# Kernel optimization log

Measured on AMD Instinct MI355X. Metric: run time of the kernel, lower is better.

The kernel has to match this reference:

```python
import jax, jax.numpy as jnp
import numpy as np

B, S, D_MODEL, N_HEAD = 8, 512, 1024, 16
HEAD_DIM = D_MODEL // N_HEAD


def _pos_embed(seq_len, dim):
    # RelativeSinusoidalPositionalEmbedding(dim, padding_idx=0, init_size=1200)
    num = 1201  # init_size + 1
    half = dim // 2
    freq = np.exp(np.arange(half, dtype=np.float32) * (-np.log(10000.0) / (half - 1)))
    pos = np.arange(-((num + 1) // 2), num // 2, dtype=np.float32)  # tf.range(-num//2, num//2), python floor div
    emb = pos[:, None] * freq[None, :]
    table = np.concatenate([np.sin(emb), np.cos(emb)], axis=1).astype(np.float32)  # [num, dim]
    table[0] = 0.0  # padding_idx = 0
    origin_shift = num // 2 + 1  # 601
    idx = np.arange(-seq_len, seq_len) + origin_shift
    return jnp.asarray(table[idx])  # [2*seq_len, dim]


def setup_inputs() -> dict:
    key = jax.random.key(0)
    k1, k2, k3, k4 = jax.random.split(key, 4)
    return {
        "x": jax.random.normal(k1, (B, S, D_MODEL), dtype=jnp.float32),
        "mask": jnp.ones((B, S), dtype=jnp.int32),
        "Wqv": jax.random.normal(k2, (D_MODEL, 2 * D_MODEL), dtype=jnp.float32) * 0.02,
        "r_r_bias": jax.random.normal(k3, (N_HEAD, HEAD_DIM), dtype=jnp.float32) * 0.02,
        "r_w_bias": jax.random.normal(k4, (N_HEAD, HEAD_DIM), dtype=jnp.float32) * 0.02,
    }


def _shift(BD):
    # [b, h, s, 2s] -> [b, h, s, s] via pad-reshape trick
    b, h, s, _ = BD.shape
    zp = jnp.zeros((b, h, s, 1), BD.dtype)
    BD = jnp.concatenate([BD, zp], axis=-1).reshape(b, h, 2 * s + 1, s)
    BD = BD[:, :, :-1].reshape(b, h, s, 2 * s)
    return BD[:, :, :, s:]


def reference(x, mask, Wqv, r_r_bias, r_w_bias):
    pos = _pos_embed(S, HEAD_DIM)  # [2S, head_dim], stop-gradient constant
    qv = x @ Wqv  # [B, S, 2*D]
    q, v = jnp.split(qv, 2, axis=-1)

    def heads(t):
        return t.reshape(B, S, N_HEAD, HEAD_DIM).transpose(0, 2, 1, 3)  # bhsd

    q, k, v = heads(q), heads(x), heads(v)
    rw_q = q + r_r_bias[None, :, None, :]
    AC = jnp.einsum('bhqd,bhkd->bhqk', rw_q, k)
    D_ = jnp.einsum('hd,ld->hl', r_w_bias, pos)[None, :, None, :]  # [1, h, 1, 2S]
    B_ = jnp.einsum('bhqd,ld->bhql', q, pos)  # [b, h, S, 2S]
    BD = _shift(B_ + D_)
    attn = AC + BD  # scale=False -> divide by 1
    m = mask.astype(jnp.float32)[:, None, None, :]
    attn = attn * m - (1.0 - m) * 1e8
    attn = jax.nn.softmax(attn, axis=-1)  # dropout is identity at inference
    out = jnp.einsum('bhqk,bhkd->bhqd', attn, v)
    return out.transpose(0, 2, 1, 3).reshape(B, S, D_MODEL)
```

## Files before the change

kernel.cpp:

```cpp
#include <hip/hip_runtime.h>


using h4 = __attribute__((ext_vector_type(4))) _Float16;
using h8 = __attribute__((ext_vector_type(8))) _Float16;
using f32x4 = __attribute__((ext_vector_type(4))) float;

#define MFMA16(a, b, c) __builtin_amdgcn_mfma_f32_16x16x32_f16((a), (b), (c), 0, 0, 0)

#define GLOAD_LDS16(gp, lp)                                                        \
  __builtin_amdgcn_global_load_lds(                                                \
      (const __attribute__((address_space(1))) unsigned int*)(gp),                 \
      (__attribute__((address_space(3))) unsigned int*)(lp), 16, 0, 0)

#define L2E 1.4426950408889634f

__global__ __launch_bounds__(256) void k_prep(const float* __restrict__ x,
                                              const float* __restrict__ Wqv,
                                              _Float16* __restrict__ xh,
                                              _Float16* __restrict__ wT,
                                              _Float16* __restrict__ posP) {
  __shared__ _Float16 t[64][72];
  int bid = blockIdx.x;
  int tid = threadIdx.x;
  if (bid < 2048) {
    size_t idx = (size_t)bid * 256 + tid;
    const float* src = x + idx * 8;
    _Float16 tmp[8];
#pragma unroll
    for (int j = 0; j < 8; ++j) tmp[j] = (_Float16)src[j];
    *(h8*)(xh + idx * 8) = *(const h8*)tmp;
  } else if (bid < 2176) {
    int idx = (bid - 2048) * 256 + tid;
    int tt = idx >> 6, j = idx & 63;
    int jj = j & 31;
    float f = expf((float)jj * (-9.210340371976184f / 31.0f));
    float ang = (float)tt * f;
    posP[idx] = (_Float16)((j < 32) ? sinf(ang) : cosf(ang));
  } else {
    int b2 = bid - 2176;
    int bk = b2 & 15, bn = b2 >> 4;
    int k0 = bk * 64, n0 = bn * 64;
    int r = tid >> 2, c = (tid & 3) * 16;
    const float* src = Wqv + (size_t)(k0 + r) * 2048 + n0 + c;
#pragma unroll
    for (int j = 0; j < 16; ++j) t[r][c + j] = (_Float16)src[j];
    __syncthreads();
    _Float16 tmp[16];
#pragma unroll
    for (int j = 0; j < 16; ++j) tmp[j] = t[c + j][r];
    _Float16* dst = wT + (size_t)(n0 + r) * 1024 + k0 + c;
    *(h8*)dst = *(const h8*)tmp;
    *(h8*)(dst + 8) = *(const h8*)(tmp + 8);
  }
}

__global__ __launch_bounds__(256) void k_gemm(const _Float16* __restrict__ xh,
                                              const _Float16* __restrict__ wT,
                                              const float* __restrict__ rr,
                                              const float* __restrict__ rw,
                                              _Float16* __restrict__ qrr,
                                              _Float16* __restrict__ qrwp,
                                              _Float16* __restrict__ vT) {
  __shared__ _Float16 At[2][128 * 64];
  __shared__ _Float16 Bt[2][128 * 64];

  int bid = blockIdx.x;
  int bm = bid & 31, bn = bid >> 5;
  int tid = threadIdx.x;
  int w = tid >> 6, lane = tid & 63;
  int lr = lane & 15, lg = lane >> 4;

  auto stage = [&](int bufi, int k0) {
#pragma unroll
    for (int it = 0; it < 4; ++it) {
      int a = w * 256 + it * 64 + lane;
      int trow = a >> 3, c8s = (a & 7) ^ (trow & 7);
      GLOAD_LDS16(xh + (size_t)(bm * 128 + trow) * 1024 + k0 + c8s * 8,
                  &At[bufi][a * 8]);
    }
#pragma unroll
    for (int it = 0; it < 4; ++it) {
      int a = w * 256 + it * 64 + lane;
      int trow = a >> 3, c8s = (a & 7) ^ (trow & 7);
      GLOAD_LDS16(wT + (size_t)(bn * 128 + trow) * 1024 + k0 + c8s * 8,
                  &Bt[bufi][a * 8]);
    }
  };

  int wm = w >> 1, wn = w & 1;
  f32x4 acc[4][4] = {};

  stage(0, 0);
  __syncthreads();
  int buf = 0;
  for (int i = 0; i < 16; ++i) {
    if (i < 15) stage(buf ^ 1, (i + 1) * 64);
#pragma unroll
    for (int kk = 0; kk < 2; ++kk) {
      h8 af[4], bf[4];
#pragma unroll
      for (int mi = 0; mi < 4; ++mi) {
        int row = wm * 64 + mi * 16 + lr;
        af[mi] = *(const h8*)(&At[buf][row * 64 + (((kk * 4 + lg) ^ (lr & 7)) * 8)]);
      }
#pragma unroll
      for (int ni = 0; ni < 4; ++ni) {
        int row = wn * 64 + ni * 16 + lr;
        bf[ni] = *(const h8*)(&Bt[buf][row * 64 + (((kk * 4 + lg) ^ (lr & 7)) * 8)]);
      }
#pragma unroll
      for (int mi = 0; mi < 4; ++mi)
#pragma unroll
        for (int ni = 0; ni < 4; ++ni)
          acc[mi][ni] = MFMA16(af[mi], bf[ni], acc[mi][ni]);
    }
    __syncthreads();
    buf ^= 1;
  }

  int hg = bn * 2 + wn;
  int mb = bm * 128 + wm * 64;
  if (hg < 16) {
    int h = hg;
    float rrv[4], rwv[4];
#pragma unroll
    for (int ni = 0; ni < 4; ++ni) {
      rrv[ni] = rr[h * 64 + ni * 16 + lr];
      rwv[ni] = rw[h * 64 + ni * 16 + lr];
    }
    float f0 = expf((float)lr * (-9.210340371976184f / 31.0f));
    float f1 = expf((float)(16 + lr) * (-9.210340371976184f / 31.0f));
#pragma unroll
    for (int mi = 0; mi < 4; ++mi)
#pragma unroll
      for (int r = 0; r < 4; ++r) {
        int m = mb + mi * 16 + lg * 4 + r;
        int b = m >> 9, s = m & 511;
        size_t base = ((size_t)(b * 16 + h) * 512 + s) * 64;
#pragma unroll
        for (int ni = 0; ni < 4; ++ni)
          qrr[base + ni * 16 + lr] = (_Float16)((acc[mi][ni][r] + rrv[ni]) * L2E);
        {
          float qs = acc[mi][0][r] + rwv[0], qc = acc[mi][2][r] + rwv[2];
          float sn, cs;
          __sincosf((float)s * f0, &sn, &cs);
          qrwp[base + lr] = (_Float16)((qs * cs + qc * sn) * L2E);
          qrwp[base + lr + 32] = (_Float16)((qc * cs - qs * sn) * L2E);
        }
        {
          float qs = acc[mi][1][r] + rwv[1], qc = acc[mi][3][r] + rwv[3];
          float sn, cs;
          __sincosf((float)s * f1, &sn, &cs);
          qrwp[base + 16 + lr] = (_Float16)((qs * cs + qc * sn) * L2E);
          qrwp[base + 16 + lr + 32] = (_Float16)((qc * cs - qs * sn) * L2E);
        }
      }
  } else {
    int h = hg - 16;
#pragma unroll
    for (int mi = 0; mi < 4; ++mi) {
      int m = mb + mi * 16 + lg * 4;
      int b = m >> 9, s0 = m & 511;
      size_t vtbase = (size_t)(b * 16 + h) * 64 * 512;
#pragma unroll
      for (int ni = 0; ni < 4; ++ni) {
        int d = ni * 16 + lr;
        _Float16 t4[4];
#pragma unroll
        for (int r = 0; r < 4; ++r) t4[r] = (_Float16)acc[mi][ni][r];
        *(h4*)(vT + vtbase + (size_t)d * 512 + s0) = *(const h4*)t4;
      }
    }
  }
}

__global__ __launch_bounds__(256, 2) void k_attn(const _Float16* __restrict__ xh,
                                                 const _Float16* __restrict__ qrr,
                                                 const _Float16* __restrict__ qrwp,
                                                 const _Float16* __restrict__ vT,
                                                 const _Float16* __restrict__ posPg,
                                                 const int* __restrict__ mask,
                                                 float* __restrict__ out) {
  __shared__ _Float16 Kp[128 * 128];
  __shared__ _Float16 Vt[64 * 128];
  __shared__ _Float16 Pl[4][16 * 136];
  __shared__ float Ma[512];

  int bid = blockIdx.x;
  int qb = bid >> 7, h = bid & 15, b = (bid >> 4) & 7;
  int q0 = qb * 128;
  int tid = threadIdx.x;
  int w = tid >> 6, lane = tid & 63;
  int lr = lane & 15, lg = lane >> 4;

  const size_t bh = (size_t)(b * 16 + h);
  const _Float16* kb = xh + (size_t)b * 512 * 1024 + h * 64;
  const _Float16* vTp = vT + bh * 64 * 512;
  const int* mrow = mask + b * 512;

  auto stage = [&](int t0s) {
#pragma unroll
    for (int it = 0; it < 8; ++it) {
      int a = w * 512 + it * 64 + lane;
      int trow = a >> 4, c16 = a & 15;
      int c16s = c16 ^ (trow & 15);
      const _Float16* g = (c16s < 8)
          ? kb + (size_t)(t0s + trow) * 1024 + c16s * 8
          : posPg + (size_t)(t0s + trow) * 64 + (c16s - 8) * 8;
      GLOAD_LDS16(g, &Kp[(size_t)(w * 512 + it * 64) * 8]);
    }
#pragma unroll
    for (int it = 0; it < 4; ++it) {
      int a = w * 256 + it * 64 + lane;
      int drow = a >> 4, c16 = a & 15;
      int c16s = c16 ^ (drow & 15);
      const _Float16* g = vTp + (size_t)drow * 512 + t0s + c16s * 8;
      GLOAD_LDS16(g, &Vt[(size_t)(w * 256 + it * 64) * 8]);
    }
  };

  Ma[tid] = (1.f - (float)mrow[tid]) * -1.4426950e8f;
  Ma[tid + 256] = (1.f - (float)mrow[tid + 256]) * -1.4426950e8f;

  h8 ar0[2], ar1[2], aw0[2], aw1[2];
#pragma unroll
  for (int rg = 0; rg < 2; ++rg) {
    const _Float16* qrr_p = qrr + (bh * 512 + q0 + 32 * w + 16 * rg + lr) * 64 + lg * 8;
    const _Float16* qrw_p = qrwp + (bh * 512 + q0 + 32 * w + 16 * rg + lr) * 64 + lg * 8;
    ar0[rg] = *(const h8*)(qrr_p);
    ar1[rg] = *(const h8*)(qrr_p + 32);
    aw0[rg] = *(const h8*)(qrw_p);
    aw1[rg] = *(const h8*)(qrw_p + 32);
  }

  float m_run[2] = {-1e30f, -1e30f}, l_run[2] = {0.f, 0.f};
  f32x4 O[2][4];
#pragma unroll
  for (int rg = 0; rg < 2; ++rg)
#pragma unroll
    for (int df = 0; df < 4; ++df) O[rg][df] = (f32x4){0.f, 0.f, 0.f, 0.f};

  _Float16* pw = &Pl[w][0];

  for (int t0 = 0; t0 < 512; t0 += 128) {
    stage(t0);
    __syncthreads();

#pragma unroll
    for (int rg = 0; rg < 2; ++rg) {
      float s[8][4];
      __builtin_amdgcn_s_setprio(1);
#pragma unroll
      for (int tf = 0; tf < 8; ++tf) {
        int row = tf * 16 + lr;
        const _Float16* bp = &Kp[row * 128];
        h8 b0 = *(const h8*)(bp + ((0 + lg) ^ lr) * 8);
        h8 b1 = *(const h8*)(bp + ((4 + lg) ^ lr) * 8);
        h8 b2 = *(const h8*)(bp + ((8 + lg) ^ lr) * 8);
        h8 b3 = *(const h8*)(bp + ((12 + lg) ^ lr) * 8);
        f32x4 c = {0.f, 0.f, 0.f, 0.f};
        c = MFMA16(b0, ar0[rg], c);
        c = MFMA16(b1, ar1[rg], c);
        c = MFMA16(b2, aw0[rg], c);
        c = MFMA16(b3, aw1[rg], c);
        f32x4 mav = *(const f32x4*)&Ma[t0 + tf * 16 + lg * 4];
#pragma unroll
        for (int r = 0; r < 4; ++r) s[tf][r] = c[r] + mav[r];
      }
      __builtin_amdgcn_s_setprio(0);

      float rm = s[0][0];
#pragma unroll
      for (int tf = 0; tf < 8; ++tf)
#pragma unroll
        for (int r = 0; r < 4; ++r) rm = fmaxf(rm, s[tf][r]);
      rm = fmaxf(rm, __shfl_xor(rm, 16));
      rm = fmaxf(rm, __shfl_xor(rm, 32));

      if (!__all(rm - m_run[rg] <= 8.f)) {
        float mn = fmaxf(m_run[rg], rm);
        float sc = exp2f(m_run[rg] - mn);
        m_run[rg] = mn;
        l_run[rg] *= sc;
        float scq[4];
#pragma unroll
        for (int r = 0; r < 4; ++r) scq[r] = __shfl(sc, lg * 4 + r);
#pragma unroll
        for (int df = 0; df < 4; ++df)
#pragma unroll
          for (int r = 0; r < 4; ++r) O[rg][df][r] *= scq[r];
      }

      float rs = 0.f;
#pragma unroll
      for (int tf = 0; tf < 8; ++tf) {
        _Float16 p4[4];
#pragma unroll
        for (int r = 0; r < 4; ++r) {
          float p = exp2f(s[tf][r] - m_run[rg]);
          p4[r] = (_Float16)p;
          rs += (float)p4[r];
        }
        *(h4*)(pw + lr * 136 + tf * 16 + lg * 4) = *(const h4*)p4;
      }
      rs += __shfl_xor(rs, 16);
      rs += __shfl_xor(rs, 32);
      l_run[rg] += rs;

      h8 pa[4];
#pragma unroll
      for (int ks = 0; ks < 4; ++ks)
        pa[ks] = *(const h8*)(pw + lr * 136 + ks * 32 + lg * 8);
      __builtin_amdgcn_s_setprio(1);
#pragma unroll
      for (int df = 0; df < 4; ++df) {
        int row = df * 16 + lr;
        const _Float16* vbp = &Vt[row * 128];
#pragma unroll
        for (int ks = 0; ks < 4; ++ks) {
          h8 vb = *(const h8*)(vbp + ((ks * 4 + lg) ^ lr) * 8);
          O[rg][df] = MFMA16(pa[ks], vb, O[rg][df]);
        }
      }
      __builtin_amdgcn_s_setprio(0);
    }
    __syncthreads();
  }

#pragma unroll
  for (int rg = 0; rg < 2; ++rg) {
    float lq[4];
#pragma unroll
    for (int r = 0; r < 4; ++r) lq[r] = __shfl(l_run[rg], lg * 4 + r);
#pragma unroll
    for (int df = 0; df < 4; ++df)
#pragma unroll
      for (int r = 0; r < 4; ++r) {
        int ii = 32 * w + 16 * rg + lg * 4 + r;
        out[((size_t)b * 512 + q0 + ii) * 1024 + h * 64 + df * 16 + lr] =
            O[rg][df][r] / lq[r];
      }
  }
}

extern "C" void kernel_launch(void* const* d_in, const int* in_sizes, int n_in,
                              void* d_out, int out_size, void* d_ws, size_t ws_size,
                              hipStream_t stream) {
  const float* x = (const float*)d_in[0];
  const int* mask = (const int*)d_in[1];
  const float* Wqv = (const float*)d_in[2];
  const float* rr = (const float*)d_in[3];
  const float* rw = (const float*)d_in[4];
  float* out = (float*)d_out;
  char* ws = (char*)d_ws;
  const size_t MB = 1024 * 1024;
  _Float16* xh = (_Float16*)(ws);
  _Float16* wT = (_Float16*)(ws + 8 * MB);
  _Float16* posP = (_Float16*)(ws + 12 * MB);
  _Float16* qrr = (_Float16*)(ws + 13 * MB);
  _Float16* qrwp = (_Float16*)(ws + 21 * MB);
  _Float16* vT = (_Float16*)(ws + 29 * MB);

  k_prep<<<2688, 256, 0, stream>>>(x, Wqv, xh, wT, posP);
  k_gemm<<<512, 256, 0, stream>>>(xh, wT, rr, rw, qrr, qrwp, vT);
  k_attn<<<512, 256, 0, stream>>>(xh, qrr, qrwp, vT, posP, mask, out);
}
```

Measured before the change: 67.74 us.

## Halve attention query tile, read V straight from global, raise occupancy

The attention kernel now gives each block 64 query rows instead of 128, so each wave handles one 16-row group. The grid doubles to 1024 blocks and launch bounds ask for 3 blocks per CU. The V tile is no longer staged in LDS; each wave loads its V fragments from global memory into registers, which frees LDS so more blocks can be resident. In exchange, every K/pos tile is staged into LDS for half as many queries, and each wave reads the full V tile on its own, which adds redundant global and cache traffic.

Result: slower. 111.9 us (+65.3%).

```diff
diff --git a/kernel.cpp b/kernel.cpp
--- a/kernel.cpp
+++ b/kernel.cpp
@@ -174,7 +174,7 @@
   }
 }
 
-__global__ __launch_bounds__(256, 2) void k_attn(const _Float16* __restrict__ xh,
+__global__ __launch_bounds__(256, 3) void k_attn(const _Float16* __restrict__ xh,
                                                  const _Float16* __restrict__ qrr,
                                                  const _Float16* __restrict__ qrwp,
                                                  const _Float16* __restrict__ vT,
@@ -182,13 +182,12 @@
                                                  const int* __restrict__ mask,
                                                  float* __restrict__ out) {
   __shared__ _Float16 Kp[128 * 128];
-  __shared__ _Float16 Vt[64 * 128];
   __shared__ _Float16 Pl[4][16 * 136];
   __shared__ float Ma[512];
 
   int bid = blockIdx.x;
   int qb = bid >> 7, h = bid & 15, b = (bid >> 4) & 7;
-  int q0 = qb * 128;
+  int q0 = qb * 64;
   int tid = threadIdx.x;
   int w = tid >> 6, lane = tid & 63;
   int lr = lane & 15, lg = lane >> 4;
@@ -209,36 +208,22 @@
           : posPg + (size_t)(t0s + trow) * 64 + (c16s - 8) * 8;
       GLOAD_LDS16(g, &Kp[(size_t)(w * 512 + it * 64) * 8]);
     }
-#pragma unroll
-    for (int it = 0; it < 4; ++it) {
-      int a = w * 256 + it * 64 + lane;
-      int drow = a >> 4, c16 = a & 15;
-      int c16s = c16 ^ (drow & 15);
-      const _Float16* g = vTp + (size_t)drow * 512 + t0s + c16s * 8;
-      GLOAD_LDS16(g, &Vt[(size_t)(w * 256 + it * 64) * 8]);
-    }
   };
 
   Ma[tid] = (1.f - (float)mrow[tid]) * -1.4426950e8f;
   Ma[tid + 256] = (1.f - (float)mrow[tid + 256]) * -1.4426950e8f;
 
-  h8 ar0[2], ar1[2], aw0[2], aw1[2];
-#pragma unroll
-  for (int rg = 0; rg < 2; ++rg) {
-    const _Float16* qrr_p = qrr + (bh * 512 + q0 + 32 * w + 16 * rg + lr) * 64 + lg * 8;
-    const _Float16* qrw_p = qrwp + (bh * 512 + q0 + 32 * w + 16 * rg + lr) * 64 + lg * 8;
-    ar0[rg] = *(const h8*)(qrr_p);
-    ar1[rg] = *(const h8*)(qrr_p + 32);
-    aw0[rg] = *(const h8*)(qrw_p);
-    aw1[rg] = *(const h8*)(qrw_p + 32);
-  }
-
-  float m_run[2] = {-1e30f, -1e30f}, l_run[2] = {0.f, 0.f};
-  f32x4 O[2][4];
-#pragma unroll
-  for (int rg = 0; rg < 2; ++rg)
-#pragma unroll
-    for (int df = 0; df < 4; ++df) O[rg][df] = (f32x4){0.f, 0.f, 0.f, 0.f};
+  const _Float16* qrr_p = qrr + (bh * 512 + q0 + 16 * w + lr) * 64 + lg * 8;
+  const _Float16* qrw_p = qrwp + (bh * 512 + q0 + 16 * w + lr) * 64 + lg * 8;
+  h8 ar0 = *(const h8*)(qrr_p);
+  h8 ar1 = *(const h8*)(qrr_p + 32);
+  h8 aw0 = *(const h8*)(qrw_p);
+  h8 aw1 = *(const h8*)(qrw_p + 32);
+
+  float m_run = -1e30f, l_run = 0.f;
+  f32x4 O[4];
+#pragma unroll
+  for (int df = 0; df < 4; ++df) O[df] = (f32x4){0.f, 0.f, 0.f, 0.f};
 
   _Float16* pw = &Pl[w][0];
 
@@ -246,101 +231,99 @@
     stage(t0);
     __syncthreads();
 
-#pragma unroll
-    for (int rg = 0; rg < 2; ++rg) {
-      float s[8][4];
-      __builtin_amdgcn_s_setprio(1);
-#pragma unroll
-      for (int tf = 0; tf < 8; ++tf) {
-        int row = tf * 16 + lr;
-        const _Float16* bp = &Kp[row * 128];
-        h8 b0 = *(const h8*)(bp + ((0 + lg) ^ lr) * 8);
-        h8 b1 = *(const h8*)(bp + ((4 + lg) ^ lr) * 8);
-        h8 b2 = *(const h8*)(bp + ((8 + lg) ^ lr) * 8);
-        h8 b3 = *(const h8*)(bp + ((12 + lg) ^ lr) * 8);
-        f32x4 c = {0.f, 0.f, 0.f, 0.f};
-        c = MFMA16(b0, ar0[rg], c);
-        c = MFMA16(b1, ar1[rg], c);
-        c = MFMA16(b2, aw0[rg], c);
-        c = MFMA16(b3, aw1[rg], c);
-        f32x4 mav = *(const f32x4*)&Ma[t0 + tf * 16 + lg * 4];
-#pragma unroll
-        for (int r = 0; r < 4; ++r) s[tf][r] = c[r] + mav[r];
-      }
-      __builtin_amdgcn_s_setprio(0);
-
-      float rm = s[0][0];
-#pragma unroll
-      for (int tf = 0; tf < 8; ++tf)
-#pragma unroll
-        for (int r = 0; r < 4; ++r) rm = fmaxf(rm, s[tf][r]);
-      rm = fmaxf(rm, __shfl_xor(rm, 16));
-      rm = fmaxf(rm, __shfl_xor(rm, 32));
-
-      if (!__all(rm - m_run[rg] <= 8.f)) {
-        float mn = fmaxf(m_run[rg], rm);
-        float sc = exp2f(m_run[rg] - mn);
-        m_run[rg] = mn;
-        l_run[rg] *= sc;
-        float scq[4];
-#pragma unroll
-        for (int r = 0; r < 4; ++r) scq[r] = __shfl(sc, lg * 4 + r);
-#pragma unroll
-        for (int df = 0; df < 4; ++df)
-#pragma unroll
-          for (int r = 0; r < 4; ++r) O[rg][df][r] *= scq[r];
-      }
-
-      float rs = 0.f;
-#pragma unroll
-      for (int tf = 0; tf < 8; ++tf) {
-        _Float16 p4[4];
-#pragma unroll
-        for (int r = 0; r < 4; ++r) {
-          float p = exp2f(s[tf][r] - m_run[rg]);
-          p4[r] = (_Float16)p;
-          rs += (float)p4[r];
-        }
-        *(h4*)(pw + lr * 136 + tf * 16 + lg * 4) = *(const h4*)p4;
-      }
-      rs += __shfl_xor(rs, 16);
-      rs += __shfl_xor(rs, 32);
-      l_run[rg] += rs;
-
-      h8 pa[4];
+    h8 vbf[4][4];
+#pragma unroll
+    for (int df = 0; df < 4; ++df) {
+      const _Float16* vp = vTp + (size_t)(df * 16 + lr) * 512 + t0 + lg * 8;
+#pragma unroll
+      for (int ks = 0; ks < 4; ++ks) vbf[df][ks] = *(const h8*)(vp + ks * 32);
+    }
+
+    float s[8][4];
+    __builtin_amdgcn_s_setprio(1);
+#pragma unroll
+    for (int tf = 0; tf < 8; ++tf) {
+      int row = tf * 16 + lr;
+      const _Float16* bp = &Kp[row * 128];
+      h8 b0 = *(const h8*)(bp + ((0 + lg) ^ lr) * 8);
+      h8 b1 = *(const h8*)(bp + ((4 + lg) ^ lr) * 8);
+      h8 b2 = *(const h8*)(bp + ((8 + lg) ^ lr) * 8);
+      h8 b3 = *(const h8*)(bp + ((12 + lg) ^ lr) * 8);
+      f32x4 c = {0.f, 0.f, 0.f, 0.f};
+      c = MFMA16(b0, ar0, c);
+      c = MFMA16(b1, ar1, c);
+      c = MFMA16(b2, aw0, c);
+      c = MFMA16(b3, aw1, c);
+      f32x4 mav = *(const f32x4*)&Ma[t0 + tf * 16 + lg * 4];
+#pragma unroll
+      for (int r = 0; r < 4; ++r) s[tf][r] = c[r] + mav[r];
+    }
+    __builtin_amdgcn_s_setprio(0);
+
+    float rm = s[0][0];
+#pragma unroll
+    for (int tf = 0; tf < 8; ++tf)
+#pragma unroll
+      for (int r = 0; r < 4; ++r) rm = fmaxf(rm, s[tf][r]);
+    rm = fmaxf(rm, __shfl_xor(rm, 16));
+    rm = fmaxf(rm, __shfl_xor(rm, 32));
+
+    if (!__all(rm - m_run <= 8.f)) {
+      float mn = fmaxf(m_run, rm);
+      float sc = exp2f(m_run - mn);
+      m_run = mn;
+      l_run *= sc;
+      float scq[4];
+#pragma unroll
+      for (int r = 0; r < 4; ++r) scq[r] = __shfl(sc, lg * 4 + r);
+#pragma unroll
+      for (int df = 0; df < 4; ++df)
+#pragma unroll
+        for (int r = 0; r < 4; ++r) O[df][r] *= scq[r];
+    }
+
+    float rs = 0.f;
+#pragma unroll
+    for (int tf = 0; tf < 8; ++tf) {
+      _Float16 p4[4];
+#pragma unroll
+      for (int r = 0; r < 4; ++r) {
+        float p = exp2f(s[tf][r] - m_run);
+        p4[r] = (_Float16)p;
+        rs += (float)p4[r];
+      }
+      *(h4*)(pw + lr * 136 + tf * 16 + lg * 4) = *(const h4*)p4;
+    }
+    rs += __shfl_xor(rs, 16);
+    rs += __shfl_xor(rs, 32);
+    l_run += rs;
+
+    h8 pa[4];
+#pragma unroll
+    for (int ks = 0; ks < 4; ++ks)
+      pa[ks] = *(const h8*)(pw + lr * 136 + ks * 32 + lg * 8);
+    __builtin_amdgcn_s_setprio(1);
+#pragma unroll
+    for (int df = 0; df < 4; ++df)
 #pragma unroll
       for (int ks = 0; ks < 4; ++ks)
-        pa[ks] = *(const h8*)(pw + lr * 136 + ks * 32 + lg * 8);
-      __builtin_amdgcn_s_setprio(1);
-#pragma unroll
-      for (int df = 0; df < 4; ++df) {
-        int row = df * 16 + lr;
-        const _Float16* vbp = &Vt[row * 128];
-#pragma unroll
-        for (int ks = 0; ks < 4; ++ks) {
-          h8 vb = *(const h8*)(vbp + ((ks * 4 + lg) ^ lr) * 8);
-          O[rg][df] = MFMA16(pa[ks], vb, O[rg][df]);
-        }
-      }
-      __builtin_amdgcn_s_setprio(0);
-    }
+        O[df] = MFMA16(pa[ks], vbf[df][ks], O[df]);
+    __builtin_amdgcn_s_setprio(0);
+
     __syncthreads();
   }
 
-#pragma unroll
-  for (int rg = 0; rg < 2; ++rg) {
-    float lq[4];
-#pragma unroll
-    for (int r = 0; r < 4; ++r) lq[r] = __shfl(l_run[rg], lg * 4 + r);
-#pragma unroll
-    for (int df = 0; df < 4; ++df)
-#pragma unroll
-      for (int r = 0; r < 4; ++r) {
-        int ii = 32 * w + 16 * rg + lg * 4 + r;
-        out[((size_t)b * 512 + q0 + ii) * 1024 + h * 64 + df * 16 + lr] =
-            O[rg][df][r] / lq[r];
-      }
-  }
+  float lq[4];
+#pragma unroll
+  for (int r = 0; r < 4; ++r) lq[r] = __shfl(l_run, lg * 4 + r);
+#pragma unroll
+  for (int df = 0; df < 4; ++df)
+#pragma unroll
+    for (int r = 0; r < 4; ++r) {
+      int ii = 16 * w + lg * 4 + r;
+      out[((size_t)b * 512 + q0 + ii) * 1024 + h * 64 + df * 16 + lr] =
+          O[df][r] / lq[r];
+    }
 }
 
 extern "C" void kernel_launch(void* const* d_in, const int* in_sizes, int n_in,
@@ -363,5 +346,5 @@
 
   k_prep<<<2688, 256, 0, stream>>>(x, Wqv, xh, wT, posP);
   k_gemm<<<512, 256, 0, stream>>>(xh, wT, rr, rw, qrr, qrwp, vT);
-  k_attn<<<512, 256, 0, stream>>>(xh, qrr, qrwp, vT, posP, mask, out);
+  k_attn<<<1024, 256, 0, stream>>>(xh, qrr, qrwp, vT, posP, mask, out);
 }
```
